# Kernel optimization log

Hardware: AMD Instinct MI355X
Metric: run time of the kernel (lower is better)

Reference implementation:

```python
import jax, jax.numpy as jnp
import numpy as np

N = 50000
E = 800000


def gcn_conv(x, W, b, src, dst, n_nodes):
    # PyG GCNConv: add self-loops, symmetric deg^-1/2 normalization,
    # out[dst] += norm * (x @ W)[src], then bias.
    h = x @ W  # [N, out]
    src_sl = jnp.concatenate([src, jnp.arange(n_nodes, dtype=src.dtype)])
    dst_sl = jnp.concatenate([dst, jnp.arange(n_nodes, dtype=dst.dtype)])
    deg = jax.ops.segment_sum(jnp.ones_like(dst_sl, dtype=h.dtype), dst_sl,
                              num_segments=n_nodes)  # in-degree incl. self-loop
    dinv = jnp.where(deg > 0, jax.lax.rsqrt(deg), 0.0)
    norm = dinv[src_sl] * dinv[dst_sl]  # [E+N]
    msg = norm[:, None] * h[src_sl]  # gather + scale, [E+N, out]
    out = jax.ops.segment_sum(msg, dst_sl, num_segments=n_nodes)
    return out + b


def setup_inputs() -> dict:
    key = jax.random.key(0)
    ks = jax.random.split(key, 8)
    F, H, O = 128, 128, 64
    x = jax.random.normal(ks[0], (N, F), dtype=jnp.float32)
    edge_index = jax.random.randint(ks[1], (2, E), 0, N, dtype=jnp.int64)
    # Glorot-ish scaled weights
    W1 = jax.random.normal(ks[2], (F, H), dtype=jnp.float32) / np.sqrt(F)
    b1 = jnp.zeros((H,), dtype=jnp.float32)
    W2 = jax.random.normal(ks[3], (H, H), dtype=jnp.float32) / np.sqrt(H)
    b2 = jnp.zeros((H,), dtype=jnp.float32)
    W3 = jax.random.normal(ks[4], (H, O), dtype=jnp.float32) / np.sqrt(H)
    b3 = jnp.zeros((O,), dtype=jnp.float32)
    return {"x": x, "edge_index": edge_index, "W1": W1, "b1": b1,
            "W2": W2, "b2": b2, "W3": W3, "b3": b3}


def reference(x, edge_index, W1, b1, W2, b2, W3, b3):
    src, dst = edge_index[0], edge_index[1]
    h = gcn_conv(x, W1, b1, src, dst, N)
    h = jax.nn.elu(h)
    h = gcn_conv(h, W2, b2, src, dst, N)
    h = jax.nn.elu(h)
    h = gcn_conv(h, W3, b3, src, dst, N)
    return h
```

## Files before the change

kernel.cpp:

```cpp
#include <hip/hip_runtime.h>
#include <hip/hip_fp16.h>
#include <math.h>


#define NFEAT_IN 128
#define SCAN_CHUNK 2048
#define NSHARD 8

typedef _Float16 f16x8 __attribute__((ext_vector_type(8)));
typedef float f32x4 __attribute__((ext_vector_type(4)));

__global__ void zero_kernel(int4* __restrict__ p, int n4) {
    int i = blockIdx.x * blockDim.x + threadIdx.x;
    if (i < n4) { int4 z; z.x = z.y = z.z = z.w = 0; p[i] = z; }
}

__global__ __launch_bounds__(256) void count_kernel(const int* __restrict__ dst,
                                                    int* __restrict__ cnt,
                                                    int E, int shard_sz) {
    int shard = blockIdx.x & (NSHARD - 1);
    int blk = blockIdx.x >> 3;
    int nblk = gridDim.x >> 3;
    int lo = shard * shard_sz, hi = lo + shard_sz;
    int stride = nblk * blockDim.x;
    int E4 = E >> 2;
    for (int g = blk * blockDim.x + threadIdx.x; g < E4; g += stride) {
        int4 d = *(const int4*)&dst[g * 4];
        if (d.x >= lo && d.x < hi) atomicAdd(&cnt[d.x], 1);
        if (d.y >= lo && d.y < hi) atomicAdd(&cnt[d.y], 1);
        if (d.z >= lo && d.z < hi) atomicAdd(&cnt[d.z], 1);
        if (d.w >= lo && d.w < hi) atomicAdd(&cnt[d.w], 1);
    }
    if (blockIdx.x == 0 && threadIdx.x < (E & 3)) {
        int d = dst[(E & ~3) + threadIdx.x];
        atomicAdd(&cnt[d], 1);
    }
}

__global__ __launch_bounds__(256) void reduce_kernel(const int* __restrict__ cnt,
                                                     int* __restrict__ bsum, int n) {
    __shared__ int wtot[4];
    int b = blockIdx.x, t = threadIdx.x;
    int base = b * SCAN_CHUNK + t * 8;
    int s = 0;
    if (base + 8 <= n) {
        int4 a = *(const int4*)&cnt[base];
        int4 c = *(const int4*)&cnt[base + 4];
        s = a.x + a.y + a.z + a.w + c.x + c.y + c.z + c.w;
    } else {
        for (int i = 0; i < 8; ++i) if (base + i < n) s += cnt[base + i];
    }
    int lane = t & 63, wid = t >> 6;
    #pragma unroll
    for (int off = 32; off > 0; off >>= 1) s += __shfl_down(s, off, 64);
    if (lane == 0) wtot[wid] = s;
    __syncthreads();
    if (t == 0) bsum[b] = wtot[0] + wtot[1] + wtot[2] + wtot[3];
}

__global__ void scanb_kernel(int* __restrict__ bsum, int nb, int* __restrict__ offs,
                             int n, int2* __restrict__ esw, int E) {
    int lane = threadIdx.x;
    int v = (lane < nb) ? bsum[lane] : 0;
    int inc = v;
    #pragma unroll
    for (int off = 1; off < 64; off <<= 1) {
        int t = __shfl_up(inc, off, 64);
        if (lane >= off) inc += t;
    }
    if (lane < nb) bsum[lane] = inc - v;
    if (lane == 63) offs[n] = inc;
    if (lane < 16) { int2 z; z.x = 0; z.y = 0; esw[E + lane] = z; }
}

__global__ __launch_bounds__(256) void scan3_kernel(const int* __restrict__ cnt,
                                                    const int* __restrict__ bbase,
                                                    int* __restrict__ offs,
                                                    int* __restrict__ pos,
                                                    float* __restrict__ dinv, int n) {
    __shared__ int wtot[4];
    int b = blockIdx.x, t = threadIdx.x;
    int base = b * SCAN_CHUNK + t * 8;
    int v[8];
    #pragma unroll
    for (int i = 0; i < 8; ++i) v[i] = (base + i < n) ? cnt[base + i] : 0;
    int psum[8], s = 0;
    #pragma unroll
    for (int i = 0; i < 8; ++i) { psum[i] = s; s += v[i]; }
    int lane = t & 63, wid = t >> 6;
    int inc = s;
    #pragma unroll
    for (int off = 1; off < 64; off <<= 1) {
        int tt = __shfl_up(inc, off, 64);
        if (lane >= off) inc += tt;
    }
    if (lane == 63) wtot[wid] = inc;
    __syncthreads();
    int wb = 0;
    for (int w = 0; w < wid; ++w) wb += wtot[w];
    int tbase = bbase[b] + wb + (inc - s);
    #pragma unroll
    for (int i = 0; i < 8; ++i) {
        if (base + i < n) {
            int o = tbase + psum[i];
            offs[base + i] = o;
            pos[base + i] = o;
            dinv[base + i] = rsqrtf((float)(v[i] + 1));
        }
    }
}

__global__ __launch_bounds__(256) void fill_kernel(const int* __restrict__ src,
                                                   const int* __restrict__ dst,
                                                   int* __restrict__ pos,
                                                   const float* __restrict__ dinv,
                                                   int2* __restrict__ esw,
                                                   int E, int shard_sz) {
    int shard = blockIdx.x & (NSHARD - 1);
    int blk = blockIdx.x >> 3;
    int nblk = gridDim.x >> 3;
    int lo = shard * shard_sz;
    int hi = lo + shard_sz;
    int stride = nblk * blockDim.x;
    for (int i = blk * blockDim.x + threadIdx.x; i < E; i += stride) {
        int d = dst[i];
        if (d >= lo && d < hi) {
            int s = src[i];
            int p = atomicAdd(&pos[d], 1);
            int2 e;
            e.x = s;
            e.y = __float_as_int(dinv[s]);
            esw[p] = e;
        }
    }
}

__global__ __launch_bounds__(256) void convx_kernel(const float* __restrict__ x,
                                                    f16x8* __restrict__ Xf, int nchunk) {
    int i = blockIdx.x * blockDim.x + threadIdx.x;
    if (i >= nchunk) return;
    int m = i >> 4, kc = i & 15;
    float4 a = *(const float4*)&x[(size_t)m * 128 + kc * 8];
    float4 b = *(const float4*)&x[(size_t)m * 128 + kc * 8 + 4];
    f16x8 v;
    v[0] = (_Float16)a.x; v[1] = (_Float16)a.y; v[2] = (_Float16)a.z; v[3] = (_Float16)a.w;
    v[4] = (_Float16)b.x; v[5] = (_Float16)b.y; v[6] = (_Float16)b.z; v[7] = (_Float16)b.w;
    int kt = kc >> 2, sub = kc & 3;
    Xf[(size_t)((m >> 4) * 4 + kt) * 64 + sub * 16 + (m & 15)] = v;
}

template <int NT>
__global__ __launch_bounds__(256) void mgemm_kernel(const f16x8* __restrict__ Xf,
                                                    const float* __restrict__ W,
                                                    __half* __restrict__ Y, int mtiles) {
    constexpr int BN = NT * 16;
    __shared__ f16x8 Wf[NT * 4 * 64];
    int t = threadIdx.x;
    #pragma unroll
    for (int i = 0; i < NT; ++i) {
        int c = t + i * 256;
        int nt = c >> 8;
        int kt = (c >> 6) & 3;
        int l = c & 63;
        int n = nt * 16 + (l & 15);
        int k0 = kt * 32 + (l >> 4) * 8;
        f16x8 v;
        #pragma unroll
        for (int j = 0; j < 8; ++j) v[j] = (_Float16)W[(size_t)(k0 + j) * BN + n];
        Wf[c] = v;
    }
    __syncthreads();
    int lane = t & 63;
    int mtile = blockIdx.x * 4 + (t >> 6);
    if (mtile >= mtiles) return;
    const f16x8* xb = Xf + (size_t)mtile * 4 * 64;
    f16x8 bf[4];
    #pragma unroll
    for (int kt = 0; kt < 4; ++kt) bf[kt] = xb[kt * 64 + lane];
    f32x4 acc[NT];
    #pragma unroll
    for (int nt = 0; nt < NT; ++nt) acc[nt] = (f32x4){0.f, 0.f, 0.f, 0.f};
    #pragma unroll
    for (int kt = 0; kt < 4; ++kt) {
        #pragma unroll
        for (int nt = 0; nt < NT; ++nt) {
            f16x8 af = Wf[(nt * 4 + kt) * 64 + lane];
            acc[nt] = __builtin_amdgcn_mfma_f32_16x16x32_f16(af, bf[kt], acc[nt], 0, 0, 0);
        }
    }
    int m = mtile * 16 + (lane & 15);
    int nc0 = (lane >> 4) * 4;
    #pragma unroll
    for (int nt = 0; nt < NT; ++nt) {
        union { __half2 h2[2]; uint2 u; } pk;
        pk.h2[0] = __floats2half2_rn(acc[nt][0], acc[nt][1]);
        pk.h2[1] = __floats2half2_rn(acc[nt][2], acc[nt][3]);
        *(uint2*)&Y[(size_t)m * BN + nt * 16 + nc0] = pk.u;
    }
}

__global__ __launch_bounds__(256) void agg128_kernel(const __half* __restrict__ H,
                                                     const int* __restrict__ offs,
                                                     const int2* __restrict__ esw,
                                                     const float* __restrict__ dinv,
                                                     const float* __restrict__ bias,
                                                     uint4* __restrict__ outf, int n) {
    int lane = threadIdx.x & 63;
    int q = lane >> 4;
    int fl = lane & 15;
    int v = blockIdx.x * 4 + (threadIdx.x >> 6);
    if (v >= n) return;
    float dv = dinv[v];
    int e0 = offs[v], e1 = offs[v + 1];
    int cntE = e1 - e0;
    int nfull = cntE >> 4;
    const char* Hb = (const char*)H + fl * 16;
    float a[8];
    #pragma unroll
    for (int k = 0; k < 8; ++k) a[k] = 0.f;
    int e = e0 + q;
    for (int i = 0; i < nfull; ++i, e += 16) {
        #pragma unroll
        for (int j = 0; j < 4; ++j) {
            int2 p = esw[e + 4 * j];
            float w = __int_as_float(p.y);
            uint4 hq = *(const uint4*)(Hb + ((size_t)(unsigned)p.x << 8));
            const _Float16* hp = (const _Float16*)&hq;
            #pragma unroll
            for (int k = 0; k < 8; ++k) a[k] = fmaf((float)hp[k], w, a[k]);
        }
    }
    if (cntE & 15) {
        #pragma unroll
        for (int j = 0; j < 4; ++j) {
            int ee = e + 4 * j;
            int2 p = esw[ee];
            float w = (ee < e1) ? __int_as_float(p.y) : 0.f;
            uint4 hq = *(const uint4*)(Hb + ((size_t)(unsigned)p.x << 8));
            const _Float16* hp = (const _Float16*)&hq;
            #pragma unroll
            for (int k = 0; k < 8; ++k) a[k] = fmaf((float)hp[k], w, a[k]);
        }
    }
    #pragma unroll
    for (int m = 16; m <= 32; m <<= 1) {
        #pragma unroll
        for (int k = 0; k < 8; ++k) a[k] += __shfl_xor(a[k], m, 64);
    }
    if (q == 0) {
        uint4 hq = *(const uint4*)(Hb + ((size_t)(unsigned)v << 8));
        const _Float16* hp = (const _Float16*)&hq;
        float b[8];
        *(float4*)&b[0] = *(const float4*)&bias[fl * 8];
        *(float4*)&b[4] = *(const float4*)&bias[fl * 8 + 4];
        float r[8];
        #pragma unroll
        for (int k = 0; k < 8; ++k) {
            float t = fmaf((float)hp[k], dv, a[k]);
            r[k] = fmaf(dv, t, b[k]);
            r[k] = r[k] > 0.f ? r[k] : expm1f(r[k]);
        }
        union { __half2 h2[4]; uint4 u; } pk;
        pk.h2[0] = __floats2half2_rn(r[0], r[1]);
        pk.h2[1] = __floats2half2_rn(r[2], r[3]);
        pk.h2[2] = __floats2half2_rn(r[4], r[5]);
        pk.h2[3] = __floats2half2_rn(r[6], r[7]);
        int blockc = (v >> 4) * 4 + (fl >> 2);
        int l2 = (fl & 3) * 16 + (v & 15);
        outf[(size_t)blockc * 64 + l2] = pk.u;
    }
}

__global__ __launch_bounds__(256) void agg64_kernel(const __half* __restrict__ H,
                                                    const int* __restrict__ offs,
                                                    const int2* __restrict__ esw,
                                                    const float* __restrict__ dinv,
                                                    const float* __restrict__ bias,
                                                    float* __restrict__ out, int n) {
    int lane = threadIdx.x & 63;
    int q = lane >> 3;
    int fl = lane & 7;
    int v = blockIdx.x * 4 + (threadIdx.x >> 6);
    if (v >= n) return;
    float dv = dinv[v];
    int e0 = offs[v], e1 = offs[v + 1];
    int cntE = e1 - e0;
    int nfull = cntE >> 4;
    const char* Hb = (const char*)H + fl * 16;
    float a[8];
    #pragma unroll
    for (int k = 0; k < 8; ++k) a[k] = 0.f;
    int e = e0 + q;
    for (int i = 0; i < nfull; ++i, e += 16) {
        #pragma unroll
        for (int j = 0; j < 2; ++j) {
            int2 p = esw[e + 8 * j];
            float w = __int_as_float(p.y);
            uint4 hq = *(const uint4*)(Hb + ((size_t)(unsigned)p.x << 7));
            const _Float16* hp = (const _Float16*)&hq;
            #pragma unroll
            for (int k = 0; k < 8; ++k) a[k] = fmaf((float)hp[k], w, a[k]);
        }
    }
    if (cntE & 15) {
        #pragma unroll
        for (int j = 0; j < 2; ++j) {
            int ee = e + 8 * j;
            int2 p = esw[ee];
            float w = (ee < e1) ? __int_as_float(p.y) : 0.f;
            uint4 hq = *(const uint4*)(Hb + ((size_t)(unsigned)p.x << 7));
            const _Float16* hp = (const _Float16*)&hq;
            #pragma unroll
            for (int k = 0; k < 8; ++k) a[k] = fmaf((float)hp[k], w, a[k]);
        }
    }
    #pragma unroll
    for (int m = 8; m <= 32; m <<= 1) {
        #pragma unroll
        for (int k = 0; k < 8; ++k) a[k] += __shfl_xor(a[k], m, 64);
    }
    if (q == 0) {
        uint4 hq = *(const uint4*)(Hb + ((size_t)(unsigned)v << 7));
        const _Float16* hp = (const _Float16*)&hq;
        float b[8];
        *(float4*)&b[0] = *(const float4*)&bias[fl * 8];
        *(float4*)&b[4] = *(const float4*)&bias[fl * 8 + 4];
        float r[8];
        #pragma unroll
        for (int k = 0; k < 8; ++k) {
            float t = fmaf((float)hp[k], dv, a[k]);
            r[k] = fmaf(dv, t, b[k]);
        }
        float4 o0, o1;
        o0.x = r[0]; o0.y = r[1]; o0.z = r[2]; o0.w = r[3];
        o1.x = r[4]; o1.y = r[5]; o1.z = r[6]; o1.w = r[7];
        *(float4*)&out[(size_t)v * 64 + fl * 8] = o0;
        *(float4*)&out[(size_t)v * 64 + fl * 8 + 4] = o1;
    }
}

static inline size_t alignup(size_t x) { return (x + 255) & ~(size_t)255; }

extern "C" void kernel_launch(void* const* d_in, const int* in_sizes, int n_in,
                              void* d_out, int out_size, void* d_ws, size_t ws_size,
                              hipStream_t stream) {
    const float* x  = (const float*)d_in[0];
    const int*   ei = (const int*)d_in[1];
    const float* W1 = (const float*)d_in[2];
    const float* b1 = (const float*)d_in[3];
    const float* W2 = (const float*)d_in[4];
    const float* b2 = (const float*)d_in[5];
    const float* W3 = (const float*)d_in[6];
    const float* b3 = (const float*)d_in[7];
    float* out = (float*)d_out;

    const int N = in_sizes[0] / NFEAT_IN;
    const int E = in_sizes[1] / 2;
    const int* src = ei;
    const int* dst = ei + E;

    char* w = (char*)d_ws;
    int* cnt  = (int*)w;  w += alignup((size_t)N * sizeof(int));
    int* pos  = (int*)w;  w += alignup((size_t)N * sizeof(int));
    int* offs = (int*)w;  w += alignup((size_t)(N + 1) * sizeof(int));
    float* dinv = (float*)w; w += alignup((size_t)N * sizeof(float));
    int* bsum = (int*)w;  w += alignup((size_t)64 * sizeof(int));
    int2* esw = (int2*)w; w += alignup((size_t)(E + 16) * sizeof(int2));
    __half* fA = (__half*)w; w += alignup((size_t)N * 128 * sizeof(__half));
    __half* hB = (__half*)w; w += alignup((size_t)N * 128 * sizeof(__half));

    const int nb = (N + SCAN_CHUNK - 1) / SCAN_CHUNK;
    const int shard_sz = (N + NSHARD - 1) / NSHARD;
    const int mtiles = N / 16;

    zero_kernel<<<(N / 4 + 255) / 256, 256, 0, stream>>>((int4*)cnt, N / 4);
    count_kernel<<<NSHARD * 128, 256, 0, stream>>>(dst, cnt, E, shard_sz);
    reduce_kernel<<<nb, 256, 0, stream>>>(cnt, bsum, N);
    scanb_kernel<<<1, 64, 0, stream>>>(bsum, nb, offs, N, esw, E);
    scan3_kernel<<<nb, 256, 0, stream>>>(cnt, bsum, offs, pos, dinv, N);
    fill_kernel<<<NSHARD * 128, 256, 0, stream>>>(src, dst, pos, dinv, esw, E, shard_sz);

    convx_kernel<<<(N * 16 + 255) / 256, 256, 0, stream>>>(x, (f16x8*)fA, N * 16);

    int gemm_grid = (mtiles + 3) / 4;
    int agg_grid = (N + 3) / 4;

    mgemm_kernel<8><<<gemm_grid, 256, 0, stream>>>((const f16x8*)fA, W1, hB, mtiles);
    agg128_kernel<<<agg_grid, 256, 0, stream>>>(hB, offs, esw, dinv, b1, (uint4*)fA, N);
    mgemm_kernel<8><<<gemm_grid, 256, 0, stream>>>((const f16x8*)fA, W2, hB, mtiles);
    agg128_kernel<<<agg_grid, 256, 0, stream>>>(hB, offs, esw, dinv, b2, (uint4*)fA, N);
    mgemm_kernel<4><<<gemm_grid, 256, 0, stream>>>((const f16x8*)fA, W3, hB, mtiles);
    agg64_kernel<<<agg_grid, 256, 0, stream>>>(hB, offs, esw, dinv, b3, out, N);
}
```

Measured before the change: 236.1 us.

## Store GEMM output column-chunked and split aggregation per 16-feature chunk

The GEMM now writes its fp16 output as 16-column chunks stored contiguously per chunk, each N×16 (32-byte rows). Aggregation launches one block group per chunk, so each chunk's gather working set is small and more likely to stay in cache. The edge list shrinks from (src, weight) pairs to src only, and the weight dinv[s] is looked up at aggregation time. The cost is more blocks, repeated reads of offsets and indices per chunk, and narrower 8-byte gathers.

```diff
diff --git a/kernel.cpp b/kernel.cpp
--- a/kernel.cpp
+++ b/kernel.cpp
@@ -59,7 +59,7 @@
 }
 
 __global__ void scanb_kernel(int* __restrict__ bsum, int nb, int* __restrict__ offs,
-                             int n, int2* __restrict__ esw, int E) {
+                             int n, int* __restrict__ srcs, int E) {
     int lane = threadIdx.x;
     int v = (lane < nb) ? bsum[lane] : 0;
     int inc = v;
@@ -70,7 +70,7 @@
     }
     if (lane < nb) bsum[lane] = inc - v;
     if (lane == 63) offs[n] = inc;
-    if (lane < 16) { int2 z; z.x = 0; z.y = 0; esw[E + lane] = z; }
+    if (lane < 16) srcs[E + lane] = 0;
 }
 
 __global__ __launch_bounds__(256) void scan3_kernel(const int* __restrict__ cnt,
@@ -113,8 +113,7 @@
 __global__ __launch_bounds__(256) void fill_kernel(const int* __restrict__ src,
                                                    const int* __restrict__ dst,
                                                    int* __restrict__ pos,
-                                                   const float* __restrict__ dinv,
-                                                   int2* __restrict__ esw,
+                                                   int* __restrict__ srcs,
                                                    int E, int shard_sz) {
     int shard = blockIdx.x & (NSHARD - 1);
     int blk = blockIdx.x >> 3;
@@ -125,12 +124,8 @@
     for (int i = blk * blockDim.x + threadIdx.x; i < E; i += stride) {
         int d = dst[i];
         if (d >= lo && d < hi) {
-            int s = src[i];
             int p = atomicAdd(&pos[d], 1);
-            int2 e;
-            e.x = s;
-            e.y = __float_as_int(dinv[s]);
-            esw[p] = e;
+            srcs[p] = src[i];
         }
     }
 }
@@ -152,7 +147,8 @@
 template <int NT>
 __global__ __launch_bounds__(256) void mgemm_kernel(const f16x8* __restrict__ Xf,
                                                     const float* __restrict__ W,
-                                                    __half* __restrict__ Y, int mtiles) {
+                                                    __half* __restrict__ Y,
+                                                    int mtiles, int nn) {
     constexpr int BN = NT * 16;
     __shared__ f16x8 Wf[NT * 4 * 64];
     int t = threadIdx.x;
@@ -195,147 +191,139 @@
         union { __half2 h2[2]; uint2 u; } pk;
         pk.h2[0] = __floats2half2_rn(acc[nt][0], acc[nt][1]);
         pk.h2[1] = __floats2half2_rn(acc[nt][2], acc[nt][3]);
-        *(uint2*)&Y[(size_t)m * BN + nt * 16 + nc0] = pk.u;
-    }
-}
-
-__global__ __launch_bounds__(256) void agg128_kernel(const __half* __restrict__ H,
+        *(uint2*)&Y[((size_t)nt * nn + m) * 16 + nc0] = pk.u;
+    }
+}
+
+__global__ __launch_bounds__(256) void agg128c_kernel(const __half* __restrict__ Hc,
+                                                      const int* __restrict__ offs,
+                                                      const int* __restrict__ srcs,
+                                                      const float* __restrict__ dinv,
+                                                      const float* __restrict__ bias,
+                                                      __half* __restrict__ outF,
+                                                      int n, int nn) {
+    int c = blockIdx.x & 7;
+    int g = blockIdx.x >> 3;
+    int t = threadIdx.x;
+    int lane = t & 63;
+    int v = g * 4 + (t >> 6);
+    if (v >= n) return;
+    int slot = lane >> 2;
+    int fq = lane & 3;
+    const char* Hb = (const char*)(Hc + (size_t)c * nn * 16) + fq * 8;
+    float dv = dinv[v];
+    int e0 = offs[v], e1 = offs[v + 1];
+    int cnt = e1 - e0;
+    int nfull = cnt >> 4;
+    float a0 = 0.f, a1 = 0.f, a2 = 0.f, a3 = 0.f;
+    int e = e0 + slot;
+    for (int i = 0; i < nfull; ++i, e += 16) {
+        int s = srcs[e];
+        float w = dinv[s];
+        uint2 hq = *(const uint2*)(Hb + ((size_t)(unsigned)s << 5));
+        const _Float16* hp = (const _Float16*)&hq;
+        a0 = fmaf((float)hp[0], w, a0);
+        a1 = fmaf((float)hp[1], w, a1);
+        a2 = fmaf((float)hp[2], w, a2);
+        a3 = fmaf((float)hp[3], w, a3);
+    }
+    if (cnt & 15) {
+        int s = srcs[e];
+        float w = (e < e1) ? dinv[s] : 0.f;
+        uint2 hq = *(const uint2*)(Hb + ((size_t)(unsigned)s << 5));
+        const _Float16* hp = (const _Float16*)&hq;
+        a0 = fmaf((float)hp[0], w, a0);
+        a1 = fmaf((float)hp[1], w, a1);
+        a2 = fmaf((float)hp[2], w, a2);
+        a3 = fmaf((float)hp[3], w, a3);
+    }
+    #pragma unroll
+    for (int m = 4; m <= 32; m <<= 1) {
+        a0 += __shfl_xor(a0, m, 64);
+        a1 += __shfl_xor(a1, m, 64);
+        a2 += __shfl_xor(a2, m, 64);
+        a3 += __shfl_xor(a3, m, 64);
+    }
+    if (slot == 0) {
+        uint2 hq = *(const uint2*)(Hb + ((size_t)(unsigned)v << 5));
+        const _Float16* hp = (const _Float16*)&hq;
+        float4 bb = *(const float4*)&bias[c * 16 + fq * 4];
+        float r0 = fmaf(dv, fmaf((float)hp[0], dv, a0), bb.x);
+        float r1 = fmaf(dv, fmaf((float)hp[1], dv, a1), bb.y);
+        float r2 = fmaf(dv, fmaf((float)hp[2], dv, a2), bb.z);
+        float r3 = fmaf(dv, fmaf((float)hp[3], dv, a3), bb.w);
+        r0 = r0 > 0.f ? r0 : expm1f(r0);
+        r1 = r1 > 0.f ? r1 : expm1f(r1);
+        r2 = r2 > 0.f ? r2 : expm1f(r2);
+        r3 = r3 > 0.f ? r3 : expm1f(r3);
+        union { __half2 h2[2]; uint2 u; } pk;
+        pk.h2[0] = __floats2half2_rn(r0, r1);
+        pk.h2[1] = __floats2half2_rn(r2, r3);
+        size_t off = ((size_t)((v >> 4) * 4 + (c >> 1)) * 64 +
+                      ((c & 1) * 2 + (fq >> 1)) * 16 + (v & 15)) * 8 + (fq & 1) * 4;
+        *(uint2*)&outF[off] = pk.u;
+    }
+}
+
+__global__ __launch_bounds__(256) void agg64c_kernel(const __half* __restrict__ Hc,
                                                      const int* __restrict__ offs,
-                                                     const int2* __restrict__ esw,
+                                                     const int* __restrict__ srcs,
                                                      const float* __restrict__ dinv,
                                                      const float* __restrict__ bias,
-                                                     uint4* __restrict__ outf, int n) {
-    int lane = threadIdx.x & 63;
-    int q = lane >> 4;
-    int fl = lane & 15;
-    int v = blockIdx.x * 4 + (threadIdx.x >> 6);
+                                                     float* __restrict__ out,
+                                                     int n, int nn) {
+    int c = blockIdx.x & 3;
+    int g = blockIdx.x >> 2;
+    int t = threadIdx.x;
+    int lane = t & 63;
+    int v = g * 4 + (t >> 6);
     if (v >= n) return;
+    int slot = lane >> 2;
+    int fq = lane & 3;
+    const char* Hb = (const char*)(Hc + (size_t)c * nn * 16) + fq * 8;
     float dv = dinv[v];
     int e0 = offs[v], e1 = offs[v + 1];
-    int cntE = e1 - e0;
-    int nfull = cntE >> 4;
-    const char* Hb = (const char*)H + fl * 16;
-    float a[8];
-    #pragma unroll
-    for (int k = 0; k < 8; ++k) a[k] = 0.f;
-    int e = e0 + q;
+    int cnt = e1 - e0;
+    int nfull = cnt >> 4;
+    float a0 = 0.f, a1 = 0.f, a2 = 0.f, a3 = 0.f;
+    int e = e0 + slot;
     for (int i = 0; i < nfull; ++i, e += 16) {
-        #pragma unroll
-        for (int j = 0; j < 4; ++j) {
-            int2 p = esw[e + 4 * j];
-            float w = __int_as_float(p.y);
-            uint4 hq = *(const uint4*)(Hb + ((size_t)(unsigned)p.x << 8));
-            const _Float16* hp = (const _Float16*)&hq;
-            #pragma unroll
-            for (int k = 0; k < 8; ++k) a[k] = fmaf((float)hp[k], w, a[k]);
-        }
-    }
-    if (cntE & 15) {
-        #pragma unroll
-        for (int j = 0; j < 4; ++j) {
-            int ee = e + 4 * j;
-            int2 p = esw[ee];
-            float w = (ee < e1) ? __int_as_float(p.y) : 0.f;
-            uint4 hq = *(const uint4*)(Hb + ((size_t)(unsigned)p.x << 8));
-            const _Float16* hp = (const _Float16*)&hq;
-            #pragma unroll
-            for (int k = 0; k < 8; ++k) a[k] = fmaf((float)hp[k], w, a[k]);
-        }
-    }
-    #pragma unroll
-    for (int m = 16; m <= 32; m <<= 1) {
-        #pragma unroll
-        for (int k = 0; k < 8; ++k) a[k] += __shfl_xor(a[k], m, 64);
-    }
-    if (q == 0) {
-        uint4 hq = *(const uint4*)(Hb + ((size_t)(unsigned)v << 8));
-        const _Float16* hp = (const _Float16*)&hq;
-        float b[8];
-        *(float4*)&b[0] = *(const float4*)&bias[fl * 8];
-        *(float4*)&b[4] = *(const float4*)&bias[fl * 8 + 4];
-        float r[8];
-        #pragma unroll
-        for (int k = 0; k < 8; ++k) {
-            float t = fmaf((float)hp[k], dv, a[k]);
-            r[k] = fmaf(dv, t, b[k]);
-            r[k] = r[k] > 0.f ? r[k] : expm1f(r[k]);
-        }
-        union { __half2 h2[4]; uint4 u; } pk;
-        pk.h2[0] = __floats2half2_rn(r[0], r[1]);
-        pk.h2[1] = __floats2half2_rn(r[2], r[3]);
-        pk.h2[2] = __floats2half2_rn(r[4], r[5]);
-        pk.h2[3] = __floats2half2_rn(r[6], r[7]);
-        int blockc = (v >> 4) * 4 + (fl >> 2);
-        int l2 = (fl & 3) * 16 + (v & 15);
-        outf[(size_t)blockc * 64 + l2] = pk.u;
-    }
-}
-
-__global__ __launch_bounds__(256) void agg64_kernel(const __half* __restrict__ H,
-                                                    const int* __restrict__ offs,
-                                                    const int2* __restrict__ esw,
-                                                    const float* __restrict__ dinv,
-                                                    const float* __restrict__ bias,
-                                                    float* __restrict__ out, int n) {
-    int lane = threadIdx.x & 63;
-    int q = lane >> 3;
-    int fl = lane & 7;
-    int v = blockIdx.x * 4 + (threadIdx.x >> 6);
-    if (v >= n) return;
-    float dv = dinv[v];
-    int e0 = offs[v], e1 = offs[v + 1];
-    int cntE = e1 - e0;
-    int nfull = cntE >> 4;
-    const char* Hb = (const char*)H + fl * 16;
-    float a[8];
-    #pragma unroll
-    for (int k = 0; k < 8; ++k) a[k] = 0.f;
-    int e = e0 + q;
-    for (int i = 0; i < nfull; ++i, e += 16) {
-        #pragma unroll
-        for (int j = 0; j < 2; ++j) {
-            int2 p = esw[e + 8 * j];
-            float w = __int_as_float(p.y);
-            uint4 hq = *(const uint4*)(Hb + ((size_t)(unsigned)p.x << 7));
-            const _Float16* hp = (const _Float16*)&hq;
-            #pragma unroll
-            for (int k = 0; k < 8; ++k) a[k] = fmaf((float)hp[k], w, a[k]);
-        }
-    }
-    if (cntE & 15) {
-        #pragma unroll
-        for (int j = 0; j < 2; ++j) {
-            int ee = e + 8 * j;
-            int2 p = esw[ee];
-            float w = (ee < e1) ? __int_as_float(p.y) : 0.f;
-            uint4 hq = *(const uint4*)(Hb + ((size_t)(unsigned)p.x << 7));
-            const _Float16* hp = (const _Float16*)&hq;
-            #pragma unroll
-            for (int k = 0; k < 8; ++k) a[k] = fmaf((float)hp[k], w, a[k]);
-        }
-    }
-    #pragma unroll
-    for (int m = 8; m <= 32; m <<= 1) {
-        #pragma unroll
-        for (int k = 0; k < 8; ++k) a[k] += __shfl_xor(a[k], m, 64);
-    }
-    if (q == 0) {
-        uint4 hq = *(const uint4*)(Hb + ((size_t)(unsigned)v << 7));
-        const _Float16* hp = (const _Float16*)&hq;
-        float b[8];
-        *(float4*)&b[0] = *(const float4*)&bias[fl * 8];
-        *(float4*)&b[4] = *(const float4*)&bias[fl * 8 + 4];
-        float r[8];
-        #pragma unroll
-        for (int k = 0; k < 8; ++k) {
-            float t = fmaf((float)hp[k], dv, a[k]);
-            r[k] = fmaf(dv, t, b[k]);
-        }
-        float4 o0, o1;
-        o0.x = r[0]; o0.y = r[1]; o0.z = r[2]; o0.w = r[3];
-        o1.x = r[4]; o1.y = r[5]; o1.z = r[6]; o1.w = r[7];
-        *(float4*)&out[(size_t)v * 64 + fl * 8] = o0;
-        *(float4*)&out[(size_t)v * 64 + fl * 8 + 4] = o1;
+        int s = srcs[e];
+        float w = dinv[s];
+        uint2 hq = *(const uint2*)(Hb + ((size_t)(unsigned)s << 5));
+        const _Float16* hp = (const _Float16*)&hq;
+        a0 = fmaf((float)hp[0], w, a0);
+        a1 = fmaf((float)hp[1], w, a1);
+        a2 = fmaf((float)hp[2], w, a2);
+        a3 = fmaf((float)hp[3], w, a3);
+    }
+    if (cnt & 15) {
+        int s = srcs[e];
+        float w = (e < e1) ? dinv[s] : 0.f;
+        uint2 hq = *(const uint2*)(Hb + ((size_t)(unsigned)s << 5));
+        const _Float16* hp = (const _Float16*)&hq;
+        a0 = fmaf((float)hp[0], w, a0);
+        a1 = fmaf((float)hp[1], w, a1);
+        a2 = fmaf((float)hp[2], w, a2);
+        a3 = fmaf((float)hp[3], w, a3);
+    }
+    #pragma unroll
+    for (int m = 4; m <= 32; m <<= 1) {
+        a0 += __shfl_xor(a0, m, 64);
+        a1 += __shfl_xor(a1, m, 64);
+        a2 += __shfl_xor(a2, m, 64);
+        a3 += __shfl_xor(a3, m, 64);
+    }
+    if (slot == 0) {
+        uint2 hq = *(const uint2*)(Hb + ((size_t)(unsigned)v << 5));
+        const _Float16* hp = (const _Float16*)&hq;
+        float4 bb = *(const float4*)&bias[c * 16 + fq * 4];
+        float4 o;
+        o.x = fmaf(dv, fmaf((float)hp[0], dv, a0), bb.x);
+        o.y = fmaf(dv, fmaf((float)hp[1], dv, a1), bb.y);
+        o.z = fmaf(dv, fmaf((float)hp[2], dv, a2), bb.z);
+        o.w = fmaf(dv, fmaf((float)hp[3], dv, a3), bb.w);
+        *(float4*)&out[(size_t)v * 64 + c * 16 + fq * 4] = o;
     }
 }
 
@@ -365,7 +353,7 @@
     int* offs = (int*)w;  w += alignup((size_t)(N + 1) * sizeof(int));
     float* dinv = (float*)w; w += alignup((size_t)N * sizeof(float));
     int* bsum = (int*)w;  w += alignup((size_t)64 * sizeof(int));
-    int2* esw = (int2*)w; w += alignup((size_t)(E + 16) * sizeof(int2));
+    int* srcs = (int*)w;  w += alignup((size_t)(E + 16) * sizeof(int));
     __half* fA = (__half*)w; w += alignup((size_t)N * 128 * sizeof(__half));
     __half* hB = (__half*)w; w += alignup((size_t)N * 128 * sizeof(__half));
 
@@ -376,19 +364,20 @@
     zero_kernel<<<(N / 4 + 255) / 256, 256, 0, stream>>>((int4*)cnt, N / 4);
     count_kernel<<<NSHARD * 128, 256, 0, stream>>>(dst, cnt, E, shard_sz);
     reduce_kernel<<<nb, 256, 0, stream>>>(cnt, bsum, N);
-    scanb_kernel<<<1, 64, 0, stream>>>(bsum, nb, offs, N, esw, E);
+    scanb_kernel<<<1, 64, 0, stream>>>(bsum, nb, offs, N, srcs, E);
     scan3_kernel<<<nb, 256, 0, stream>>>(cnt, bsum, offs, pos, dinv, N);
-    fill_kernel<<<NSHARD * 128, 256, 0, stream>>>(src, dst, pos, dinv, esw, E, shard_sz);
+    fill_kernel<<<NSHARD * 128, 256, 0, stream>>>(src, dst, pos, srcs, E, shard_sz);
 
     convx_kernel<<<(N * 16 + 255) / 256, 256, 0, stream>>>(x, (f16x8*)fA, N * 16);
 
     int gemm_grid = (mtiles + 3) / 4;
-    int agg_grid = (N + 3) / 4;
-
-    mgemm_kernel<8><<<gemm_grid, 256, 0, stream>>>((const f16x8*)fA, W1, hB, mtiles);
-    agg128_kernel<<<agg_grid, 256, 0, stream>>>(hB, offs, esw, dinv, b1, (uint4*)fA, N);
-    mgemm_kernel<8><<<gemm_grid, 256, 0, stream>>>((const f16x8*)fA, W2, hB, mtiles);
-    agg128_kernel<<<agg_grid, 256, 0, stream>>>(hB, offs, esw, dinv, b2, (uint4*)fA, N);
-    mgemm_kernel<4><<<gemm_grid, 256, 0, stream>>>((const f16x8*)fA, W3, hB, mtiles);
-    agg64_kernel<<<agg_grid, 256, 0, stream>>>(hB, offs, esw, dinv, b3, out, N);
-}
+    int agg128_grid = (N / 4) * 8;
+    int agg64_grid = (N / 4) * 4;
+
+    mgemm_kernel<8><<<gemm_grid, 256, 0, stream>>>((const f16x8*)fA, W1, hB, mtiles, N);
+    agg128c_kernel<<<agg128_grid, 256, 0, stream>>>(hB, offs, srcs, dinv, b1, fA, N, N);
+    mgemm_kernel<8><<<gemm_grid, 256, 0, stream>>>((const f16x8*)fA, W2, hB, mtiles, N);
+    agg128c_kernel<<<agg128_grid, 256, 0, stream>>>(hB, offs, srcs, dinv, b2, fA, N, N);
+    mgemm_kernel<4><<<gemm_grid, 256, 0, stream>>>((const f16x8*)fA, W3, hB, mtiles, N);
+    agg64c_kernel<<<agg64_grid, 256, 0, stream>>>(hB, offs, srcs, dinv, b3, out, N, N);
+}
```

Result: slower. 444.6 us (+88.3%).
